# Performance work log

Hardware: AMD Instinct MI355X
Metric: run time of the kernel (lower is better)

Reference implementation:

```python
import jax, jax.numpy as jnp
import numpy as np

N, E, G = 200000, 1200000, 2048
NODE_DIM, H = 5, 64
NEG_SLOPE = 0.2


def setup_inputs() -> dict:
    key = jax.random.key(0)
    ks = jax.random.split(key, 20)
    def glorot(k, shape):
        fan = sum(shape) if len(shape) > 1 else shape[0] + 1
        return jax.random.normal(k, shape, jnp.float32) * jnp.sqrt(2.0 / fan)
    inp = {
        'x': jax.random.normal(ks[0], (N, NODE_DIM), jnp.float32),
        'edge_index': jax.random.randint(ks[1], (2, E), 0, N, jnp.int64),
        'batch': jnp.sort(jax.random.randint(ks[2], (N,), 0, G, jnp.int64)),
        'embed_W': glorot(ks[3], (NODE_DIM, H)), 'embed_b': jnp.zeros((H,), jnp.float32),
        'g1_W': glorot(ks[4], (H, H)), 'g1_asrc': glorot(ks[5], (H,)), 'g1_adst': glorot(ks[6], (H,)), 'g1_b': jnp.zeros((H,), jnp.float32),
        'g2_W': glorot(ks[7], (H, H)), 'g2_asrc': glorot(ks[8], (H,)), 'g2_adst': glorot(ks[9], (H,)), 'g2_b': jnp.zeros((H,), jnp.float32),
        'fc1_W': glorot(ks[10], (2 * H, 64)), 'fc1_b': jnp.zeros((64,), jnp.float32),
        'fc2_W': glorot(ks[11], (64, 32)), 'fc2_b': jnp.zeros((32,), jnp.float32),
        'fc3_W': glorot(ks[12], (32, 1)), 'fc3_b': jnp.zeros((1,), jnp.float32),
    }
    return inp


def gat_conv(x, src, dst, W, a_src, a_dst, b):
    # x: [N, H] -> h: [N, H]; edges (with self-loops) src->dst
    h = x @ W
    alpha_s = h @ a_src  # [N]
    alpha_d = h @ a_dst  # [N]
    e = jax.nn.leaky_relu(alpha_s[src] + alpha_d[dst], NEG_SLOPE)  # [E']
    m = jax.ops.segment_max(e, dst, num_segments=N)
    w = jnp.exp(e - m[dst])
    denom = jax.ops.segment_sum(w, dst, num_segments=N)
    alpha = w / (denom[dst] + 1e-16)
    out = jax.ops.segment_sum(h[src] * alpha[:, None], dst, num_segments=N)
    return out + b


def reference(x, edge_index, batch, embed_W, embed_b,
              g1_W, g1_asrc, g1_adst, g1_b,
              g2_W, g2_asrc, g2_adst, g2_b,
              fc1_W, fc1_b, fc2_W, fc2_b, fc3_W, fc3_b):
    # add self loops once (PyG GATConv default add_self_loops=True)
    loops = jnp.arange(N, dtype=edge_index.dtype)
    src = jnp.concatenate([edge_index[0], loops])
    dst = jnp.concatenate([edge_index[1], loops])

    h = x @ embed_W + embed_b
    h = gat_conv(h, src, dst, g1_W, g1_asrc, g1_adst, g1_b)
    h = jax.nn.relu(h)
    h = gat_conv(h, src, dst, g2_W, g2_asrc, g2_adst, g2_b)

    # global mean / max pooling per graph
    cnt = jax.ops.segment_sum(jnp.ones((N,), h.dtype), batch, num_segments=G)
    mean = jax.ops.segment_sum(h, batch, num_segments=G) / jnp.maximum(cnt, 1.0)[:, None]
    mx = jax.ops.segment_max(h, batch, num_segments=G)
    mx = jnp.where(cnt[:, None] > 0, mx, 0.0)
    g = jnp.concatenate([mean, mx], axis=1)  # [G, 2H]

    g = jax.nn.relu(g @ fc1_W + fc1_b)
    g = jax.nn.relu(g @ fc2_W + fc2_b)
    return g @ fc3_W + fc3_b  # [G, 1]
```

## Files before the change

### kernel.cpp

```cpp
#include <hip/hip_runtime.h>
#include <hip/hip_bf16.h>
#include <hip/hip_fp16.h>

#define HD 64
#define NODE_DIM 5
#define NEG_SLOPE 0.2f
#define GT 64
#define BSH 9
#define BNODES 512
#define NBMAX 512
#define BCAP 4096
#define EPB 8
#define LDH 72

typedef _Float16 f16x8 __attribute__((ext_vector_type(8)));
typedef float f32x4 __attribute__((ext_vector_type(4)));

template <bool EMBED>
__global__ __launch_bounds__(256) void gemm_alpha_k(
    const void* __restrict__ hin, const float* __restrict__ embW,
    const float* __restrict__ embB, const float* __restrict__ W,
    const float* __restrict__ asrc, const float* __restrict__ adst,
    __half* __restrict__ hout, float* __restrict__ alpha_s,
    float* __restrict__ alpha_d, int* __restrict__ bcnt0, int N) {
    __shared__ _Float16 hs[GT * LDH];
    __shared__ _Float16 Wt[HD * LDH];
    __shared__ float xe[GT * NODE_DIM];
    __shared__ float we[NODE_DIM * HD + HD];
    const int t = threadIdx.x;
    const int n0 = blockIdx.x * GT;
    if (EMBED && blockIdx.x == 0) {
        for (int j = t; j < NBMAX; j += 256) bcnt0[j] = 0;
    }
    if (n0 >= N) return;
    const int rem = N - n0;

#pragma unroll
    for (int j = 0; j < 16; j++) {
        int idx = t + 256 * j;
        int k = idx >> 6, n = idx & 63;
        Wt[n * LDH + k] = (_Float16)W[idx];
    }

    if (EMBED) {
        const float* xin = (const float*)hin;
        for (int j = t; j < GT * NODE_DIM; j += 256)
            xe[j] = (j < rem * NODE_DIM) ? xin[(size_t)n0 * NODE_DIM + j] : 0.0f;
        for (int j = t; j < NODE_DIM * HD + HD; j += 256)
            we[j] = (j < NODE_DIM * HD) ? embW[j] : embB[j - NODE_DIM * HD];
        __syncthreads();
        int r = t >> 2, d0 = (t & 3) * 16;
#pragma unroll
        for (int jj = 0; jj < 16; jj++) {
            int d = d0 + jj;
            float acc = we[NODE_DIM * HD + d];
#pragma unroll
            for (int k = 0; k < NODE_DIM; k++)
                acc = fmaf(xe[r * NODE_DIM + k], we[k * HD + d], acc);
            hs[r * LDH + d] = (r < rem) ? (_Float16)acc : (_Float16)0.0f;
        }
    } else {
        const short4* g4 = (const short4*)((const __half*)hin + (size_t)n0 * HD);
#pragma unroll
        for (int j = 0; j < 4; j++) {
            int idx = t + 256 * j;
            int row = idx >> 4, c4 = idx & 15;
            short4 v = {0, 0, 0, 0};
            if (row < rem) v = g4[idx];
            *(short4*)(hs + row * LDH + c4 * 4) = v;
        }
    }
    __syncthreads();

    const int lane = t & 63;
    const int w = t >> 6;
    const int r16 = lane & 15;
    const int g = lane >> 4;

    const _Float16* hrow = hs + (w * 16 + r16) * LDH + g * 8;
    f16x8 b0 = *(const f16x8*)(hrow);
    f16x8 b1 = *(const f16x8*)(hrow + 32);

    f32x4 acc[4];
#pragma unroll
    for (int mt = 0; mt < 4; mt++) acc[mt] = (f32x4){0.f, 0.f, 0.f, 0.f};

#pragma unroll
    for (int mt = 0; mt < 4; mt++) {
        const _Float16* arow = Wt + (mt * 16 + r16) * LDH + g * 8;
        f16x8 a0 = *(const f16x8*)(arow);
        f16x8 a1 = *(const f16x8*)(arow + 32);
        acc[mt] = __builtin_amdgcn_mfma_f32_16x16x32_f16(a0, b0, acc[mt], 0, 0, 0);
        acc[mt] = __builtin_amdgcn_mfma_f32_16x16x32_f16(a1, b1, acc[mt], 0, 0, 0);
    }

    const int node = n0 + w * 16 + r16;
    float ps = 0.0f, pd = 0.0f;
    if (node < N) {
#pragma unroll
        for (int mt = 0; mt < 4; mt++) {
            float4 av = ((const float4*)asrc)[mt * 4 + g];
            float4 bv = ((const float4*)adst)[mt * 4 + g];
            ps += acc[mt][0] * av.x + acc[mt][1] * av.y +
                  acc[mt][2] * av.z + acc[mt][3] * av.w;
            pd += acc[mt][0] * bv.x + acc[mt][1] * bv.y +
                  acc[mt][2] * bv.z + acc[mt][3] * bv.w;
            short4 s;
            s.x = __half_as_short(__float2half_rn(acc[mt][0]));
            s.y = __half_as_short(__float2half_rn(acc[mt][1]));
            s.z = __half_as_short(__float2half_rn(acc[mt][2]));
            s.w = __half_as_short(__float2half_rn(acc[mt][3]));
            ((short4*)hout)[(size_t)node * 16 + mt * 4 + g] = s;
        }
    }
    ps += __shfl_xor(ps, 16);
    ps += __shfl_xor(ps, 32);
    pd += __shfl_xor(pd, 16);
    pd += __shfl_xor(pd, 32);
    if (g == 0 && node < N) {
        alpha_s[node] = ps;
        alpha_d[node] = pd;
    }
}


__global__ __launch_bounds__(256) void partition_k(
    const int* __restrict__ ei, int* __restrict__ bcnt,
    int* __restrict__ bpack, int E) {
    __shared__ int lcnt[NBMAX], lbase[NBMAX];
    int dst[EPB], src[EPB];
    int jb = blockIdx.x * (256 * EPB) + threadIdx.x;
#pragma unroll
    for (int u = 0; u < EPB; u++) {
        int j = jb + u * 256;
        if (j < E) {
            dst[u] = __builtin_nontemporal_load(&ei[E + j]);
            src[u] = __builtin_nontemporal_load(&ei[j]);
        } else dst[u] = -1;
    }
    for (int b = threadIdx.x; b < NBMAX; b += 256) lcnt[b] = 0;
    __syncthreads();
#pragma unroll
    for (int u = 0; u < EPB; u++)
        if (dst[u] >= 0) atomicAdd(&lcnt[dst[u] >> BSH], 1);
    __syncthreads();
    for (int b = threadIdx.x; b < NBMAX; b += 256) {
        int c = lcnt[b];
        lbase[b] = c ? (b * BCAP + atomicAdd(&bcnt[b], c)) : 0;
        lcnt[b] = 0;
    }
    __syncthreads();
#pragma unroll
    for (int u = 0; u < EPB; u++) {
        if (dst[u] >= 0) {
            int b = dst[u] >> BSH;
            int o = atomicAdd(&lcnt[b], 1);
            bpack[lbase[b] + o] = (src[u] << BSH) | (dst[u] & (BNODES - 1));
        }
    }
}

__global__ __launch_bounds__(256) void bucket_csr_k(
    const int* __restrict__ bpack, const int* __restrict__ bcnt,
    int* __restrict__ off, int* __restrict__ csr_src, int N, int NB) {
    __shared__ int s[BNODES];
    __shared__ int lcur[BNODES];
    __shared__ int sred[256];
    const int t = threadIdx.x;
    const int b = blockIdx.x;
    const int nbase = b << BSH;
    const int cnt = bcnt[b];
    const int w0 = b * BCAP;

    int part = 0;
    for (int j = t; j < b; j += 256) part += bcnt[j];
    sred[t] = part;
    s[t] = 0; s[t + 256] = 0;
    __syncthreads();
#pragma unroll
    for (int o = 128; o; o >>= 1) {
        if (t < o) sred[t] += sred[t + o];
        __syncthreads();
    }
    const int e0 = sred[0];

    for (int j = t; j < cnt; j += 256)
        atomicAdd(&s[bpack[w0 + j] & (BNODES - 1)], 1);
    __syncthreads();
    int d0 = s[t], d1 = s[t + 256];
#pragma unroll
    for (int o = 1; o < BNODES; o <<= 1) {
        int a0 = (t >= o) ? s[t - o] : 0;
        int a1 = (t + 256 >= o) ? s[t + 256 - o] : 0;
        __syncthreads();
        s[t] += a0;
        s[t + 256] += a1;
        __syncthreads();
    }
    int ex0 = s[t] - d0, ex1 = s[t + 256] - d1;
    lcur[t] = ex0; lcur[t + 256] = ex1;
    int n0 = nbase + t, n1 = nbase + t + 256;
    if (n0 < N) off[n0] = e0 + ex0;
    if (n1 < N) off[n1] = e0 + ex1;
    if (t == 0 && b == NB - 1) off[N] = e0 + cnt;
    __syncthreads();
    for (int j = t; j < cnt; j += 256) {
        int v = bpack[w0 + j];
        int pos = atomicAdd(&lcur[v & (BNODES - 1)], 1);
        csr_src[e0 + pos] = v >> BSH;
    }
}

template <bool BR>
__global__ __launch_bounds__(256) void gather_k(
    const int* __restrict__ off, const int* __restrict__ csr_src,
    const float* __restrict__ as, const float* __restrict__ ad,
    const __half* __restrict__ h, const float* __restrict__ bias,
    __half* __restrict__ out, int N) {
    int tid = blockIdx.x * blockDim.x + threadIdx.x;
    int wv = tid >> 6;
    int lane = threadIdx.x & 63;
    int grp = lane >> 4;
    int l16 = lane & 15;
    int n = wv * 4 + grp;
    if (n >= N) return;
    int s0 = off[n], s1 = off[n + 1];
    float adv = ad[n];
    const short4* h4 = (const short4*)h;

    float e = as[n] + adv;
    e = (e >= 0.0f) ? e : NEG_SLOPE * e;
    float wsl = __expf(e);
    float l0 = wsl, l1 = 0.0f;
    short4 hvs = h4[(unsigned)(n * 16 + l16)];
    float4 acc0, acc1 = {0, 0, 0, 0};
    acc0.x = wsl * __half2float(__short_as_half(hvs.x));
    acc0.y = wsl * __half2float(__short_as_half(hvs.y));
    acc0.z = wsl * __half2float(__short_as_half(hvs.z));
    acc0.w = wsl * __half2float(__short_as_half(hvs.w));

    int i = s0;
    for (; i + 4 <= s1; i += 4) {
        int src0 = csr_src[i], src1 = csr_src[i + 1];
        int src2 = csr_src[i + 2], src3 = csr_src[i + 3];
        float e0 = as[src0] + adv, e1 = as[src1] + adv;
        float e2 = as[src2] + adv, e3 = as[src3] + adv;
        short4 hv0 = h4[(unsigned)(src0 * 16 + l16)];
        short4 hv1 = h4[(unsigned)(src1 * 16 + l16)];
        short4 hv2 = h4[(unsigned)(src2 * 16 + l16)];
        short4 hv3 = h4[(unsigned)(src3 * 16 + l16)];
        e0 = (e0 >= 0.0f) ? e0 : NEG_SLOPE * e0;
        e1 = (e1 >= 0.0f) ? e1 : NEG_SLOPE * e1;
        e2 = (e2 >= 0.0f) ? e2 : NEG_SLOPE * e2;
        e3 = (e3 >= 0.0f) ? e3 : NEG_SLOPE * e3;
        float w0 = __expf(e0), w1 = __expf(e1), w2 = __expf(e2), w3 = __expf(e3);
        l0 += w0 + w2; l1 += w1 + w3;
        acc0.x = fmaf(w0, __half2float(__short_as_half(hv0.x)), acc0.x);
        acc0.y = fmaf(w0, __half2float(__short_as_half(hv0.y)), acc0.y);
        acc0.z = fmaf(w0, __half2float(__short_as_half(hv0.z)), acc0.z);
        acc0.w = fmaf(w0, __half2float(__short_as_half(hv0.w)), acc0.w);
        acc1.x = fmaf(w1, __half2float(__short_as_half(hv1.x)), acc1.x);
        acc1.y = fmaf(w1, __half2float(__short_as_half(hv1.y)), acc1.y);
        acc1.z = fmaf(w1, __half2float(__short_as_half(hv1.z)), acc1.z);
        acc1.w = fmaf(w1, __half2float(__short_as_half(hv1.w)), acc1.w);
        acc0.x = fmaf(w2, __half2float(__short_as_half(hv2.x)), acc0.x);
        acc0.y = fmaf(w2, __half2float(__short_as_half(hv2.y)), acc0.y);
        acc0.z = fmaf(w2, __half2float(__short_as_half(hv2.z)), acc0.z);
        acc0.w = fmaf(w2, __half2float(__short_as_half(hv2.w)), acc0.w);
        acc1.x = fmaf(w3, __half2float(__short_as_half(hv3.x)), acc1.x);
        acc1.y = fmaf(w3, __half2float(__short_as_half(hv3.y)), acc1.y);
        acc1.z = fmaf(w3, __half2float(__short_as_half(hv3.z)), acc1.z);
        acc1.w = fmaf(w3, __half2float(__short_as_half(hv3.w)), acc1.w);
    }
    for (; i + 2 <= s1; i += 2) {
        int src0 = csr_src[i], src1 = csr_src[i + 1];
        float e0 = as[src0] + adv;
        float e1 = as[src1] + adv;
        short4 hv0 = h4[(unsigned)(src0 * 16 + l16)];
        short4 hv1 = h4[(unsigned)(src1 * 16 + l16)];
        e0 = (e0 >= 0.0f) ? e0 : NEG_SLOPE * e0;
        e1 = (e1 >= 0.0f) ? e1 : NEG_SLOPE * e1;
        float w0 = __expf(e0), w1 = __expf(e1);
        l0 += w0; l1 += w1;
        acc0.x = fmaf(w0, __half2float(__short_as_half(hv0.x)), acc0.x);
        acc0.y = fmaf(w0, __half2float(__short_as_half(hv0.y)), acc0.y);
        acc0.z = fmaf(w0, __half2float(__short_as_half(hv0.z)), acc0.z);
        acc0.w = fmaf(w0, __half2float(__short_as_half(hv0.w)), acc0.w);
        acc1.x = fmaf(w1, __half2float(__short_as_half(hv1.x)), acc1.x);
        acc1.y = fmaf(w1, __half2float(__short_as_half(hv1.y)), acc1.y);
        acc1.z = fmaf(w1, __half2float(__short_as_half(hv1.z)), acc1.z);
        acc1.w = fmaf(w1, __half2float(__short_as_half(hv1.w)), acc1.w);
    }
    if (i < s1) {
        int src0 = csr_src[i];
        float e0 = as[src0] + adv;
        short4 hv0 = h4[(unsigned)(src0 * 16 + l16)];
        e0 = (e0 >= 0.0f) ? e0 : NEG_SLOPE * e0;
        float w0 = __expf(e0);
        l0 += w0;
        acc0.x = fmaf(w0, __half2float(__short_as_half(hv0.x)), acc0.x);
        acc0.y = fmaf(w0, __half2float(__short_as_half(hv0.y)), acc0.y);
        acc0.z = fmaf(w0, __half2float(__short_as_half(hv0.z)), acc0.z);
        acc0.w = fmaf(w0, __half2float(__short_as_half(hv0.w)), acc0.w);
    }
    float inv = 1.0f / (l0 + l1 + 1e-16f);
    float4 r;
    r.x = (acc0.x + acc1.x) * inv;
    r.y = (acc0.y + acc1.y) * inv;
    r.z = (acc0.z + acc1.z) * inv;
    r.w = (acc0.w + acc1.w) * inv;
    if (BR) {
        float4 b = ((const float4*)bias)[l16];
        r.x = fmaxf(r.x + b.x, 0.0f);
        r.y = fmaxf(r.y + b.y, 0.0f);
        r.z = fmaxf(r.z + b.z, 0.0f);
        r.w = fmaxf(r.w + b.w, 0.0f);
    }
    short4 o;
    o.x = __half_as_short(__float2half_rn(r.x));
    o.y = __half_as_short(__float2half_rn(r.y));
    o.z = __half_as_short(__float2half_rn(r.z));
    o.w = __half_as_short(__float2half_rn(r.w));
    ((short4*)out)[(unsigned)(n * 16 + l16)] = o;
}

__global__ __launch_bounds__(256) void pool_mlp_k(
    const __half* __restrict__ hfin, const float* __restrict__ hb,
    const int* __restrict__ batch, int N,
    const float* __restrict__ fc1W, const float* __restrict__ fc1b,
    const float* __restrict__ fc2W, const float* __restrict__ fc2b,
    const float* __restrict__ fc3W, const float* __restrict__ fc3b,
    float* __restrict__ out) {
    __shared__ float psum[16][64];
    __shared__ float pmax[16][64];
    __shared__ float lds[192];
    int g = blockIdx.x;
    int t = threadIdx.x;
    int gg = t >> 4;
    int l16 = t & 15;
    int lo = 0, hi = N;
    while (lo < hi) { int mid = (lo + hi) >> 1; if (batch[mid] < g) lo = mid + 1; else hi = mid; }
    int start = lo;
    lo = start; hi = N;
    while (lo < hi) { int mid = (lo + hi) >> 1; if (batch[mid] < g + 1) lo = mid + 1; else hi = mid; }
    int end = lo;
    const short4* h4 = (const short4*)hfin;
    float4 sum = {0, 0, 0, 0};
    float4 mx = {-INFINITY, -INFINITY, -INFINITY, -INFINITY};
    for (int n = start + gg; n < end; n += 16) {
        short4 v = h4[(size_t)n * 16 + l16];
        float a = __half2float(__short_as_half(v.x));
        float b = __half2float(__short_as_half(v.y));
        float c = __half2float(__short_as_half(v.z));
        float d = __half2float(__short_as_half(v.w));
        sum.x += a; sum.y += b; sum.z += c; sum.w += d;
        mx.x = fmaxf(mx.x, a); mx.y = fmaxf(mx.y, b);
        mx.z = fmaxf(mx.z, c); mx.w = fmaxf(mx.w, d);
    }
    *(float4*)&psum[gg][l16 * 4] = sum;
    *(float4*)&pmax[gg][l16 * 4] = mx;
    __syncthreads();
    if (t < 64) {
        float s = 0.0f, m = -INFINITY;
#pragma unroll
        for (int k = 0; k < 16; k++) {
            s += psum[k][t];
            m = fmaxf(m, pmax[k][t]);
        }
        int cnt = end - start;
        float bias = hb[t];
        lds[t]      = (cnt > 0) ? s / (float)cnt + bias : 0.0f;
        lds[64 + t] = (cnt > 0) ? m + bias : 0.0f;
    }
    __syncthreads();
    if (t < 64) {
        int lane = t;
        float o1 = fc1b[lane];
        for (int k = 0; k < 128; k++) o1 += lds[k] * fc1W[k * 64 + lane];
        o1 = fmaxf(o1, 0.0f);
        __builtin_amdgcn_s_barrier();
        lds[128 + lane] = o1;
        float o2 = 0.0f;
        if (lane < 32) {
            o2 = fc2b[lane];
            for (int k = 0; k < 64; k++) o2 += lds[128 + k] * fc2W[k * 32 + lane];
            o2 = fmaxf(o2, 0.0f);
        }
        float part = (lane < 32) ? o2 * fc3W[lane] : 0.0f;
#pragma unroll
        for (int off = 32; off; off >>= 1) part += __shfl_xor(part, off);
        if (lane == 0) out[g] = part + fc3b[0];
    }
}

static inline size_t align256(size_t x) { return (x + 255) & ~(size_t)255; }

extern "C" void kernel_launch(void* const* d_in, const int* in_sizes, int n_in,
                              void* d_out, int out_size, void* d_ws, size_t ws_size,
                              hipStream_t stream) {
    const float* x      = (const float*)d_in[0];
    const int*   ei     = (const int*)d_in[1];
    const int*   batch  = (const int*)d_in[2];
    const float* embW   = (const float*)d_in[3];
    const float* embB   = (const float*)d_in[4];
    const float* g1W    = (const float*)d_in[5];
    const float* g1as   = (const float*)d_in[6];
    const float* g1ad   = (const float*)d_in[7];
    const float* g1b    = (const float*)d_in[8];
    const float* g2W    = (const float*)d_in[9];
    const float* g2as   = (const float*)d_in[10];
    const float* g2ad   = (const float*)d_in[11];
    const float* g2b    = (const float*)d_in[12];
    const float* fc1W   = (const float*)d_in[13];
    const float* fc1b   = (const float*)d_in[14];
    const float* fc2W   = (const float*)d_in[15];
    const float* fc2b   = (const float*)d_in[16];
    const float* fc3W   = (const float*)d_in[17];
    const float* fc3b   = (const float*)d_in[18];
    float* out = (float*)d_out;

    const int N  = in_sizes[0] / NODE_DIM;
    const int E  = in_sizes[1] / 2;
    const int G  = out_size;
    const int NH = N * HD;
    const int NB = (N + BNODES - 1) >> BSH;

    char* ws = (char*)d_ws;
    __half* bufA    = (__half*)ws; ws += align256((size_t)NH * 2);
    __half* bufB    = (__half*)ws; ws += align256((size_t)NH * 2);
    float*  as_buf  = (float*)ws;  ws += align256((size_t)N * 4);
    float*  ad_buf  = (float*)ws;  ws += align256((size_t)N * 4);
    int*    off     = (int*)ws;    ws += align256((size_t)(N + 1) * 4);
    int*    bcnt    = (int*)ws;    ws += align256((size_t)NBMAX * 4);
    int*    bpack   = (int*)ws;    ws += align256((size_t)NB * BCAP * 4);
    int*    csrsrc  = (int*)ws;    ws += align256((size_t)E * 4);

    const int B = 256;
    dim3 blk(B);
    dim3 gr_gemm((N + GT - 1) / GT);
    dim3 gr_gath(((N + 3) / 4 * 64 + B - 1) / B);
    dim3 gr_epb((E + B * EPB - 1) / (B * EPB));

    gemm_alpha_k<true><<<gr_gemm, blk, 0, stream>>>(x, embW, embB, g1W, g1as, g1ad,
                                                    bufB, as_buf, ad_buf, bcnt, N);
    partition_k<<<gr_epb, blk, 0, stream>>>(ei, bcnt, bpack, E);
    bucket_csr_k<<<dim3(NB), blk, 0, stream>>>(bpack, bcnt, off, csrsrc, N, NB);

    gather_k<true><<<gr_gath, blk, 0, stream>>>(off, csrsrc, as_buf, ad_buf,
                                                bufB, g1b, bufA, N);

    gemm_alpha_k<false><<<gr_gemm, blk, 0, stream>>>(bufA, nullptr, nullptr, g2W,
                                                     g2as, g2ad, bufB, as_buf, ad_buf,
                                                     nullptr, N);
    gather_k<false><<<gr_gath, blk, 0, stream>>>(off, csrsrc, as_buf, ad_buf,
                                                 bufB, nullptr, bufA, N);

    pool_mlp_k<<<dim3(G), dim3(256), 0, stream>>>(bufA, g2b, batch, N,
                                                  fc1W, fc1b, fc2W, fc2b, fc3W, fc3b, out);
}
```

Measured before the change: 265.0 us.

## Sort nodes by in-degree within buckets to balance gather wavefront work

The CSR build kernel now counting-sorts the nodes of each 512-node bucket by in-degree (capped at 63) and writes a permutation array. Both gather kernels process nodes in that permuted order, so the four 16-lane groups in a wavefront get nodes of similar degree and idle less from divergence. The cost is an extra indirection load per node, scattered output writes, and less locality in h/off accesses.

```diff
diff --git a/kernel.cpp b/kernel.cpp
--- a/kernel.cpp
+++ b/kernel.cpp
@@ -162,10 +162,13 @@
 
 __global__ __launch_bounds__(256) void bucket_csr_k(
     const int* __restrict__ bpack, const int* __restrict__ bcnt,
-    int* __restrict__ off, int* __restrict__ csr_src, int N, int NB) {
+    int* __restrict__ off, int* __restrict__ csr_src, int* __restrict__ perm,
+    int N, int NB) {
     __shared__ int s[BNODES];
     __shared__ int lcur[BNODES];
     __shared__ int sred[256];
+    __shared__ int dbin[64];
+    __shared__ int dcur[64];
     const int t = threadIdx.x;
     const int b = blockIdx.x;
     const int nbase = b << BSH;
@@ -176,6 +179,7 @@
     for (int j = t; j < b; j += 256) part += bcnt[j];
     sred[t] = part;
     s[t] = 0; s[t + 256] = 0;
+    if (t < 64) dbin[t] = 0;
     __syncthreads();
 #pragma unroll
     for (int o = 128; o; o >>= 1) {
@@ -209,11 +213,31 @@
         int pos = atomicAdd(&lcur[v & (BNODES - 1)], 1);
         csr_src[e0 + pos] = v >> BSH;
     }
+
+    const int bin0 = min(d0, 63), bin1 = min(d1, 63);
+    const bool v0 = n0 < N, v1 = n1 < N;
+    if (v0) atomicAdd(&dbin[bin0], 1);
+    if (v1) atomicAdd(&dbin[bin1], 1);
+    __syncthreads();
+    if (t < 64) {
+        int v = dbin[t];
+        int inc = v;
+#pragma unroll
+        for (int o = 1; o < 64; o <<= 1) {
+            int u = __shfl_up(inc, o);
+            if (t >= o) inc += u;
+        }
+        dcur[t] = inc - v;
+    }
+    __syncthreads();
+    if (v0) { int p = atomicAdd(&dcur[bin0], 1); perm[nbase + p] = n0; }
+    if (v1) { int p = atomicAdd(&dcur[bin1], 1); perm[nbase + p] = n1; }
 }
 
 template <bool BR>
 __global__ __launch_bounds__(256) void gather_k(
     const int* __restrict__ off, const int* __restrict__ csr_src,
+    const int* __restrict__ perm,
     const float* __restrict__ as, const float* __restrict__ ad,
     const __half* __restrict__ h, const float* __restrict__ bias,
     __half* __restrict__ out, int N) {
@@ -222,8 +246,9 @@
     int lane = threadIdx.x & 63;
     int grp = lane >> 4;
     int l16 = lane & 15;
-    int n = wv * 4 + grp;
-    if (n >= N) return;
+    int nl = wv * 4 + grp;
+    if (nl >= N) return;
+    int n = perm[nl];
     int s0 = off[n], s1 = off[n + 1];
     float adv = ad[n];
     const short4* h4 = (const short4*)h;
@@ -432,6 +457,7 @@
     float*  ad_buf  = (float*)ws;  ws += align256((size_t)N * 4);
     int*    off     = (int*)ws;    ws += align256((size_t)(N + 1) * 4);
     int*    bcnt    = (int*)ws;    ws += align256((size_t)NBMAX * 4);
+    int*    perm    = (int*)ws;    ws += align256((size_t)N * 4);
     int*    bpack   = (int*)ws;    ws += align256((size_t)NB * BCAP * 4);
     int*    csrsrc  = (int*)ws;    ws += align256((size_t)E * 4);
 
@@ -444,15 +470,15 @@
     gemm_alpha_k<true><<<gr_gemm, blk, 0, stream>>>(x, embW, embB, g1W, g1as, g1ad,
                                                     bufB, as_buf, ad_buf, bcnt, N);
     partition_k<<<gr_epb, blk, 0, stream>>>(ei, bcnt, bpack, E);
-    bucket_csr_k<<<dim3(NB), blk, 0, stream>>>(bpack, bcnt, off, csrsrc, N, NB);
-
-    gather_k<true><<<gr_gath, blk, 0, stream>>>(off, csrsrc, as_buf, ad_buf,
+    bucket_csr_k<<<dim3(NB), blk, 0, stream>>>(bpack, bcnt, off, csrsrc, perm, N, NB);
+
+    gather_k<true><<<gr_gath, blk, 0, stream>>>(off, csrsrc, perm, as_buf, ad_buf,
                                                 bufB, g1b, bufA, N);
 
     gemm_alpha_k<false><<<gr_gemm, blk, 0, stream>>>(bufA, nullptr, nullptr, g2W,
                                                      g2as, g2ad, bufB, as_buf, ad_buf,
                                                      nullptr, N);
-    gather_k<false><<<gr_gath, blk, 0, stream>>>(off, csrsrc, as_buf, ad_buf,
+    gather_k<false><<<gr_gath, blk, 0, stream>>>(off, csrsrc, perm, as_buf, ad_buf,
                                                  bufB, nullptr, bufA, N);
 
     pool_mlp_k<<<dim3(G), dim3(256), 0, stream>>>(bufA, g2b, batch, N,
```

After: 282.3 us. 6.5% more time.
